# Kernel optimization log

Hardware: AMD Instinct MI355X
Metric: run time of the kernel (lower is better)

Reference implementation:

```python
import jax, jax.numpy as jnp
import numpy as np

TEMP = 0.3

def setup_inputs() -> dict:
    key = jax.random.key(0)
    k1, k2, k3 = jax.random.split(key, 3)
    N, d, T, Q = 2048, 256, 256, 64
    scale = 1.0 / np.sqrt(d)  # keep dot/temp in a numerically safe range for exp
    x = jax.random.normal(k1, (N, d), jnp.float32) * scale
    y = jax.random.normal(k2, (T, Q, d), jnp.float32) * scale
    track_idxs = jax.random.randint(k3, (N,), 0, T, dtype=jnp.int32)
    return {"x": x, "track_idxs": track_idxs, "y": y}


def reference(x, track_idxs, y):
    # Defaults: global_contrast=True, separate_tracks=True, static_contrast=True,
    # soft_condition=True, sim_type='dot'. Vectorized segment-sum form of the
    # per-unique-track Python loop in the original module.
    T, Q, d = y.shape
    yf = y.reshape(T * Q, d)                       # flatten(0,1): track-major
    y_idxs = jnp.tile(jnp.arange(T, dtype=jnp.int32), Q)  # torch .repeat(Q) == tile
    tid = track_idxs.astype(jnp.int32)

    S_xy = jnp.exp(x @ yf.T / TEMP)                # [N, T*Q]
    S_xx = jnp.exp(x @ x.T / TEMP)                 # [N, N]

    # Sum S columns grouped by (buggy-but-faithful) y track id / x track id -> [N, T]
    xy_by_track = jax.ops.segment_sum(S_xy.T, y_idxs, num_segments=T).T
    xx_by_track = jax.ops.segment_sum(S_xx.T, tid, num_segments=T).T

    rxy_total = S_xy.sum(axis=1)                   # [N]
    rxx_total = S_xx.sum(axis=1)                   # [N]
    rxy_pos = jnp.take_along_axis(xy_by_track, tid[:, None], axis=1)[:, 0]
    rxx_pos_full = jnp.take_along_axis(xx_by_track, tid[:, None], axis=1)[:, 0]
    rxx_pos = rxx_pos_full - jnp.diagonal(S_xx)    # exclude self-pairs (1 - eye)

    # per-row numerator/denominator contributions
    num_i = rxy_pos + 0.5 * rxx_pos                # static same-track sum halved
    den_i = (rxy_total - rxy_pos) + (rxx_total - rxx_pos_full)

    num_t = jax.ops.segment_sum(num_i, tid, num_segments=T)  # [T]
    den_t = jax.ops.segment_sum(den_i, tid, num_segments=T)
    counts = jax.ops.segment_sum(jnp.ones_like(num_i), tid, num_segments=T)
    present = counts > 0                            # unique() track ids

    num_safe = jnp.where(present, num_t, 1.0)
    den_safe = jnp.where(present, den_t, 0.0)
    loss_t = -jnp.log(num_safe / (den_safe + num_safe))  # soft_condition loss
    loss_t = jnp.where(present, loss_t, 0.0)
    n_present = present.sum().astype(loss_t.dtype)
    return (loss_t.sum() / n_present).reshape(1)
```

## Files before the change

kernel.cpp:

```cpp
#include <hip/hip_runtime.h>

#define NN   2048
#define DD   256
#define TT   256
#define NYC  16384
#define CHUNK_COLS 128
#define NCHUNK_XY 128
#define NCHUNK_XX 16
#define NROWBLK   16

static constexpr float INV_TEMP = 1.0f / 0.3f;

typedef __bf16 bf16x8 __attribute__((ext_vector_type(8)));
typedef float  f32x4  __attribute__((ext_vector_type(4)));


__global__ void cvt_zero_kernel(const float* __restrict__ x, const float* __restrict__ y,
                                bf16x8* __restrict__ xfl, bf16x8* __restrict__ yfl,
                                float* __restrict__ acc ) {
    const int tid0   = blockIdx.x * blockDim.x + threadIdx.x;
    const int stride = gridDim.x * blockDim.x;
    for (int j = tid0; j < 3 * NN; j += stride) acc[j] = 0.f;

    const int NXF = NN * DD / 8;
    for (int j = tid0; j < NXF; j += stride) {
        const int gk  = j >> 6;
        const int sub = j & 63;
        const int qq  = sub & 3;
        const int cc  = (sub >> 2) & 15;
        const int col = ((gk >> 3) << 4) + cc;
        const int k0  = ((gk & 7) << 5) + (qq << 3);
        const float4* s = (const float4*)(x + (size_t)col * DD + k0);
        float4 v0 = s[0], v1 = s[1];
        bf16x8 o;
        o[0] = (__bf16)v0.x; o[1] = (__bf16)v0.y; o[2] = (__bf16)v0.z; o[3] = (__bf16)v0.w;
        o[4] = (__bf16)v1.x; o[5] = (__bf16)v1.y; o[6] = (__bf16)v1.z; o[7] = (__bf16)v1.w;
        xfl[(size_t)gk * 64 + qq * 16 + cc] = o;
    }
    const int NYF = NYC * DD / 8;
    for (int j = tid0; j < NYF; j += stride) {
        const int gk  = j >> 6;
        const int sub = j & 63;
        const int qq  = sub & 3;
        const int cc  = (sub >> 2) & 15;
        const int col = ((gk >> 3) << 4) + cc;
        const int k0  = ((gk & 7) << 5) + (qq << 3);
        const float4* s = (const float4*)(y + (size_t)col * DD + k0);
        float4 v0 = s[0], v1 = s[1];
        bf16x8 o;
        o[0] = (__bf16)v0.x; o[1] = (__bf16)v0.y; o[2] = (__bf16)v0.z; o[3] = (__bf16)v0.w;
        o[4] = (__bf16)v1.x; o[5] = (__bf16)v1.y; o[6] = (__bf16)v1.z; o[7] = (__bf16)v1.w;
        yfl[(size_t)gk * 64 + qq * 16 + cc] = o;
    }
}

__global__ __launch_bounds__(256, 3) void stats_kernel(
        const bf16x8* __restrict__ xfl, const bf16x8* __restrict__ yfl,
        const int* __restrict__ tid,
        float* __restrict__ Tot, float* __restrict__ Pxy,
        float* __restrict__ Pxx, float* __restrict__ diag) {
    const int id    = blockIdx.x;
    const int chunk = (id & 7) + ((id >> 7) << 3);
    const int bx    = (id >> 3) & 15;
    const int mode  = (chunk >= NCHUNK_XY);
    const int colbase = (mode ? chunk - NCHUNK_XY : chunk) * CHUNK_COLS;
    const bf16x8* __restrict__ colfl = mode ? xfl : yfl;

    const int lane = threadIdx.x & 63;
    const int w    = threadIdx.x >> 6;
    const int c16  = lane & 15;
    const int q    = lane >> 4;
    const int rowbase = bx * 128 + w * 32;
    const int rowg    = rowbase >> 4;

    bf16x8 a[2][8];
#pragma unroll
    for (int t = 0; t < 2; t++)
#pragma unroll
        for (int ks = 0; ks < 8; ks++)
            a[t][ks] = xfl[((size_t)(rowg + t) * 8 + ks) * 64 + lane];

    int trow[2];
#pragma unroll
    for (int t = 0; t < 2; t++) {
        const int rb = rowbase + t * 16 + q * 4;
        trow[t] = tid[rb] | (tid[rb + 1] << 8) | (tid[rb + 2] << 16) | (tid[rb + 3] << 24);
    }

    const bf16x8* bptr = colfl + (size_t)(colbase >> 4) * 8 * 64 + lane;
    const bool wantdiag = mode && (bx == (colbase >> 7));

    float tot[2][4] = {};
    float pos[2][4] = {};

    bf16x8 b0[4], b1[4];
#pragma unroll
    for (int s = 0; s < 4; s++) b0[s] = bptr[(size_t)s * 64];

    for (int ct = 0; ct < CHUNK_COLS / 16; ct++) {
#pragma unroll
        for (int s = 0; s < 4; s++) b1[s] = bptr[((size_t)ct * 8 + 4 + s) * 64];
        const int col    = colbase + ct * 16 + c16;
        const int coltid = mode ? tid[col] : (col & (TT - 1));

        f32x4 acc[2];
#pragma unroll
        for (int t = 0; t < 2; t++) acc[t] = (f32x4){0.f, 0.f, 0.f, 0.f};

#pragma unroll
        for (int s = 0; s < 4; s++)
#pragma unroll
            for (int t = 0; t < 2; t++)
                acc[t] = __builtin_amdgcn_mfma_f32_16x16x32_bf16(a[t][s], b0[s], acc[t], 0, 0, 0);

        if (ct < CHUNK_COLS / 16 - 1) {
#pragma unroll
            for (int s = 0; s < 4; s++) b0[s] = bptr[((size_t)(ct + 1) * 8 + s) * 64];
        }

#pragma unroll
        for (int s = 0; s < 4; s++)
#pragma unroll
            for (int t = 0; t < 2; t++)
                acc[t] = __builtin_amdgcn_mfma_f32_16x16x32_bf16(a[t][4 + s], b1[s], acc[t], 0, 0, 0);

#pragma unroll
        for (int t = 0; t < 2; t++) {
            const int rw0 = rowbase + t * 16 + q * 4;
#pragma unroll
            for (int r = 0; r < 4; r++) {
                const float val = __expf(acc[t][r] * INV_TEMP);
                tot[t][r] += val;
                pos[t][r] += (((trow[t] >> (8 * r)) & 255) == coltid) ? val : 0.f;
                if (wantdiag && col == rw0 + r)
                    diag[col] = val;
            }
        }
    }

#pragma unroll
    for (int t = 0; t < 2; t++)
#pragma unroll
        for (int r = 0; r < 4; r++) {
            float aS = tot[t][r], p = pos[t][r];
#pragma unroll
            for (int off = 1; off < 16; off <<= 1) {
                aS += __shfl_xor(aS, off);
                p  += __shfl_xor(p, off);
            }
            if (c16 == 0) {
                const int row = rowbase + t * 16 + q * 4 + r;
                atomicAdd(&Tot[row], aS);
                atomicAdd(mode ? &Pxx[row] : &Pxy[row], p);
            }
        }
}

__global__ void finalize_kernel(const float* __restrict__ Tot, const float* __restrict__ Pxy,
                                const float* __restrict__ Pxx, const float* __restrict__ diag,
                                const int* __restrict__ tid, float* __restrict__ out) {
    __shared__ float num_s[TT], den_s[TT];
    __shared__ int cnt_s[TT];
    const int t = threadIdx.x;
    num_s[t] = 0.f; den_s[t] = 0.f; cnt_s[t] = 0;
    __syncthreads();
    for (int i = t; i < NN; i += 256) {
        float tt_ = Tot[i], pxy = Pxy[i], pxx = Pxx[i];
        float num = pxy + 0.5f * (pxx - diag[i]);
        float den = tt_ - pxy - pxx;
        int tr = tid[i];
        atomicAdd(&num_s[tr], num);
        atomicAdd(&den_s[tr], den);
        atomicAdd(&cnt_s[tr], 1);
    }
    __syncthreads();
    float lt = 0.f, pr = 0.f;
    if (cnt_s[t] > 0) {
        lt = -logf(num_s[t] / (den_s[t] + num_s[t]));
        pr = 1.f;
    }
    for (int off = 32; off; off >>= 1) { lt += __shfl_down(lt, off); pr += __shfl_down(pr, off); }
    __shared__ float ls[4], ps[4];
    if ((t & 63) == 0) { ls[t >> 6] = lt; ps[t >> 6] = pr; }
    __syncthreads();
    if (t == 0) out[0] = (ls[0] + ls[1] + ls[2] + ls[3]) / (ps[0] + ps[1] + ps[2] + ps[3]);
}

extern "C" void kernel_launch(void* const* d_in, const int* in_sizes, int n_in,
                              void* d_out, int out_size, void* d_ws, size_t ws_size,
                              hipStream_t stream) {
    const float* x   = (const float*)d_in[0];
    const int*   tid = (const int*)d_in[1];
    const float* y   = (const float*)d_in[2];
    float* out = (float*)d_out;

    char* ws = (char*)d_ws;
    bf16x8* xfl = (bf16x8*)ws;
    bf16x8* yfl = (bf16x8*)(ws + (1u << 20));
    float* acc  = (float*)(ws + 9u * (1u << 20));
    float* Tot  = acc;
    float* Pxy  = acc + NN;
    float* Pxx  = acc + 2 * NN;
    float* diag = acc + 3 * NN;

    cvt_zero_kernel<<<2304, 256, 0, stream>>>(x, y, xfl, yfl, acc);
    stats_kernel<<<NROWBLK * (NCHUNK_XY + NCHUNK_XX), 256, 0, stream>>>(
        xfl, yfl, tid, Tot, Pxy, Pxx, diag);
    finalize_kernel<<<1, 256, 0, stream>>>(Tot, Pxy, Pxx, diag, tid, out);
}
```

Baseline: 120.2 us.

## Stage shared B column tiles in LDS via double-buffered direct global-to-LDS loads

Each block now loads each 16-column B tile from global memory once, using global_load_lds into a two-slot LDS buffer, instead of all four waves fetching the same tile into registers. The next tile is prefetched while MFMAs run on the current one, with a block barrier every iteration. Per-column track ids are also loaded once up front rather than inside the loop. This cuts redundant global/L2 traffic and register pressure, at the cost of 16KB of LDS per block and eight barriers per block.

```diff
diff --git a/kernel.cpp b/kernel.cpp
--- a/kernel.cpp
+++ b/kernel.cpp
@@ -59,6 +59,8 @@
         const int* __restrict__ tid,
         float* __restrict__ Tot, float* __restrict__ Pxy,
         float* __restrict__ Pxx, float* __restrict__ diag) {
+    __shared__ __align__(16) char bstage[2][8192];
+
     const int id    = blockIdx.x;
     const int chunk = (id & 7) + ((id >> 7) << 3);
     const int bx    = (id >> 3) & 15;
@@ -66,8 +68,9 @@
     const int colbase = (mode ? chunk - NCHUNK_XY : chunk) * CHUNK_COLS;
     const bf16x8* __restrict__ colfl = mode ? xfl : yfl;
 
-    const int lane = threadIdx.x & 63;
-    const int w    = threadIdx.x >> 6;
+    const int tix  = threadIdx.x;
+    const int lane = tix & 63;
+    const int w    = tix >> 6;
     const int c16  = lane & 15;
     const int q    = lane >> 4;
     const int rowbase = bx * 128 + w * 32;
@@ -87,56 +90,71 @@
         trow[t] = tid[rb] | (tid[rb + 1] << 8) | (tid[rb + 2] << 16) | (tid[rb + 3] << 24);
     }
 
-    const bf16x8* bptr = colfl + (size_t)(colbase >> 4) * 8 * 64 + lane;
+    int ctid[8];
+#pragma unroll
+    for (int ct = 0; ct < 8; ct++) {
+        const int col = colbase + ct * 16 + c16;
+        ctid[ct] = mode ? tid[col] : (col & (TT - 1));
+    }
+
+    const char* gbase = (const char*)colfl + ((size_t)(colbase >> 4)) * 8192 + tix * 16;
     const bool wantdiag = mode && (bx == (colbase >> 7));
 
     float tot[2][4] = {};
     float pos[2][4] = {};
 
-    bf16x8 b0[4], b1[4];
-#pragma unroll
-    for (int s = 0; s < 4; s++) b0[s] = bptr[(size_t)s * 64];
-
-    for (int ct = 0; ct < CHUNK_COLS / 16; ct++) {
-#pragma unroll
-        for (int s = 0; s < 4; s++) b1[s] = bptr[((size_t)ct * 8 + 4 + s) * 64];
-        const int col    = colbase + ct * 16 + c16;
-        const int coltid = mode ? tid[col] : (col & (TT - 1));
-
-        f32x4 acc[2];
-#pragma unroll
-        for (int t = 0; t < 2; t++) acc[t] = (f32x4){0.f, 0.f, 0.f, 0.f};
-
-#pragma unroll
-        for (int s = 0; s < 4; s++)
-#pragma unroll
-            for (int t = 0; t < 2; t++)
-                acc[t] = __builtin_amdgcn_mfma_f32_16x16x32_bf16(a[t][s], b0[s], acc[t], 0, 0, 0);
-
-        if (ct < CHUNK_COLS / 16 - 1) {
-#pragma unroll
-            for (int s = 0; s < 4; s++) b0[s] = bptr[((size_t)(ct + 1) * 8 + s) * 64];
+#define STAGE(ct_, buf_)                                                              \
+    do {                                                                              \
+        const char* g_ = gbase + (size_t)(ct_) * 8192;                                \
+        __builtin_amdgcn_global_load_lds(                                             \
+            (const __attribute__((address_space(1))) void*)g_,                        \
+            (__attribute__((address_space(3))) void*)&bstage[buf_][tix * 16],         \
+            16, 0, 0);                                                                \
+        __builtin_amdgcn_global_load_lds(                                             \
+            (const __attribute__((address_space(1))) void*)(g_ + 4096),               \
+            (__attribute__((address_space(3))) void*)&bstage[buf_][4096 + tix * 16],  \
+            16, 0, 0);                                                                \
+    } while (0)
+
+    STAGE(0, 0);
+    __syncthreads();
+
+#pragma unroll
+    for (int ct = 0; ct < 8; ct++) {
+        if (ct < 7) STAGE(ct + 1, (ct + 1) & 1);
+        const char* lbase = &bstage[ct & 1][0];
+
+        f32x4 acc0 = {0.f, 0.f, 0.f, 0.f};
+        f32x4 acc1 = {0.f, 0.f, 0.f, 0.f};
+#pragma unroll
+        for (int h = 0; h < 2; h++) {
+            bf16x8 bf[4];
+#pragma unroll
+            for (int k = 0; k < 4; k++)
+                bf[k] = *(const bf16x8*)(lbase + (h * 4 + k) * 1024 + lane * 16);
+#pragma unroll
+            for (int k = 0; k < 4; k++) {
+                acc0 = __builtin_amdgcn_mfma_f32_16x16x32_bf16(a[0][h * 4 + k], bf[k], acc0, 0, 0, 0);
+                acc1 = __builtin_amdgcn_mfma_f32_16x16x32_bf16(a[1][h * 4 + k], bf[k], acc1, 0, 0, 0);
+            }
         }
 
-#pragma unroll
-        for (int s = 0; s < 4; s++)
-#pragma unroll
-            for (int t = 0; t < 2; t++)
-                acc[t] = __builtin_amdgcn_mfma_f32_16x16x32_bf16(a[t][4 + s], b1[s], acc[t], 0, 0, 0);
-
+        const int col = colbase + ct * 16 + c16;
 #pragma unroll
         for (int t = 0; t < 2; t++) {
+            const f32x4 acv = t ? acc1 : acc0;
             const int rw0 = rowbase + t * 16 + q * 4;
 #pragma unroll
             for (int r = 0; r < 4; r++) {
-                const float val = __expf(acc[t][r] * INV_TEMP);
+                const float val = __expf(acv[r] * INV_TEMP);
                 tot[t][r] += val;
-                pos[t][r] += (((trow[t] >> (8 * r)) & 255) == coltid) ? val : 0.f;
-                if (wantdiag && col == rw0 + r)
-                    diag[col] = val;
+                pos[t][r] += (((trow[t] >> (8 * r)) & 255) == ctid[ct]) ? val : 0.f;
+                if (wantdiag && col == rw0 + r) diag[col] = val;
             }
         }
-    }
+        __syncthreads();
+    }
+#undef STAGE
 
 #pragma unroll
     for (int t = 0; t < 2; t++)
```

Measured after the change: 113.5 us. 1.06x faster.
